# Kernel tuning notes

Hardware: AMD Instinct MI355X
Metric: run time of the kernel (lower is better)

The kernel has to match this reference:

```python
import jax, jax.numpy as jnp
import numpy as np

M, D_H, D_K, D_V = 8, 512, 64, 64
B, N = 16, 1024

def _xavier(key, shape, gain=1.414):
    fan_in, fan_out = shape[-2], shape[-1]
    limit = gain * (6.0 / (fan_in + fan_out)) ** 0.5
    return jax.random.uniform(key, shape, jnp.float32, -limit, limit)

def setup_inputs() -> dict:
    key = jax.random.key(0)
    kH, kq, kk, kv, ko = jax.random.split(key, 5)
    return {
        "H": jax.random.normal(kH, (B, N, D_H), jnp.float32),
        "W_Q": _xavier(kq, (M, D_H, D_K)),
        "W_K": _xavier(kk, (M, D_H, D_K)),
        "W_V": _xavier(kv, (M, D_H, D_V)),
        "W_O": _xavier(ko, (M, D_V, D_H)),
    }

def reference(H, W_Q, W_K, W_V, W_O):
    # H: [B, n, d_h]; per-head projections -> [B, M, n, d_k/d_v]
    Q = jnp.einsum('bnd,mdq->bmnq', H, W_Q)
    K = jnp.einsum('bnd,mdk->bmnk', H, W_K)
    V = jnp.einsum('bnd,mdv->bmnv', H, W_V)
    scale = 1.0 / jnp.sqrt(jnp.float32(W_K.shape[-1]))
    U = scale * jnp.einsum('bmnq,bmkq->bmnk', Q, K)  # [B, M, n, n]
    A = jax.nn.softmax(U, axis=-1)
    Hp = jnp.einsum('bmnk,bmkv->bmnv', A, V)          # [B, M, n, d_v]
    # per-head output projection then sum over heads (dim=-3)
    return jnp.einsum('bmnv,mvd->bnd', Hp, W_O)       # [B, n, d_h]
```

## Files before the change

kernel.cpp:

```cpp
#include <hip/hip_runtime.h>
#include <hip/hip_bf16.h>

typedef __attribute__((ext_vector_type(8))) short bf16x8;
typedef __attribute__((ext_vector_type(4))) float f32x4;
typedef __attribute__((ext_vector_type(16))) float f32x16;
typedef __attribute__((ext_vector_type(2))) unsigned uint2v;

__device__ __forceinline__ ushort f2bf(float f) {
  union { float f; unsigned u; } v; v.f = f;
  unsigned r = v.u + 0x7FFFu + ((v.u >> 16) & 1u);
  return (ushort)(r >> 16);
}

__device__ __forceinline__ float exp2_(float x) {
#if __has_builtin(__builtin_amdgcn_exp2f)
  return __builtin_amdgcn_exp2f(x);
#else
  return exp2f(x);
#endif
}

__device__ __forceinline__ unsigned cvtpk(float lo, float hi) {
  unsigned r;
  asm("v_cvt_pk_bf16_f32 %0, %1, %2" : "=v"(r) : "v"(lo), "v"(hi));
  return r;
}

__device__ __forceinline__ uint2v lane32_swap(unsigned a, unsigned b) {
#if __has_builtin(__builtin_amdgcn_permlane32_swap)
  return __builtin_amdgcn_permlane32_swap(a, b, false, false);
#else
  unsigned sa = (unsigned)__shfl_xor((int)a, 32);
  unsigned sb = (unsigned)__shfl_xor((int)b, 32);
  bool lo = ((threadIdx.x & 32) == 0);
  uint2v r;
  r.x = lo ? a : sb;
  r.y = lo ? sa : b;
  return r;
#endif
}

__device__ __forceinline__ void gload_lds16(const ushort* g, ushort* l) {
  __builtin_amdgcn_global_load_lds(
      (const __attribute__((address_space(1))) void*)g,
      (__attribute__((address_space(3))) void*)l, 16, 0, 0);
}

#define QSCALE 0.18033688011112042f

__global__ void __launch_bounds__(256) prep_kernel(
    const float* __restrict__ H, const float* __restrict__ WQ,
    const float* __restrict__ WK, const float* __restrict__ WV,
    const float* __restrict__ WO, ushort* __restrict__ Hb,
    ushort* __restrict__ Wqkv, ushort* __restrict__ Wo) {
  int bid = blockIdx.x;
  if (bid < 4096) {
    int i = (bid * 256 + threadIdx.x) * 8;
    float4 a = *(const float4*)(H + i);
    float4 b = *(const float4*)(H + i + 4);
    uint4 o;
    o.x = f2bf(a.x) | ((unsigned)f2bf(a.y) << 16);
    o.y = f2bf(a.z) | ((unsigned)f2bf(a.w) << 16);
    o.z = f2bf(b.x) | ((unsigned)f2bf(b.y) << 16);
    o.w = f2bf(b.z) | ((unsigned)f2bf(b.w) << 16);
    *(uint4*)(Hb + i) = o;
  } else if (bid < 7168) {
    int t = (bid - 4096) * 256 + threadIdx.x;
    int j = t >> 9, d = t & 511;
    int m = j / 192, r = j % 192, which = r >> 6, dk = r & 63;
    const float* W = (which == 0) ? WQ : (which == 1) ? WK : WV;
    Wqkv[t] = f2bf(W[(m * 512 + d) * 64 + dk]);
  } else {
    int t = (bid - 7168) * 256 + threadIdx.x;
    int j = t >> 9, mv = t & 511;
    Wo[t] = f2bf(WO[mv * 512 + j]);
  }
}

template <int EPI>
__global__ void __launch_bounds__(256) gemm_bt_kernel(
    const ushort* __restrict__ A, const ushort* __restrict__ Bt,
    float* __restrict__ C, int Kdim, int Ncols,
    ushort* __restrict__ Qo, ushort* __restrict__ Ko, ushort* __restrict__ Vo) {
  __shared__ __align__(16) ushort As[128 * 64];
  __shared__ __align__(16) ushort Bs[128 * 64];
  const int tid = threadIdx.x;
  const int lane = tid & 63, w = tid >> 6;
  const int wr = w >> 1, wc = w & 1;
  const int brow = blockIdx.y * 128, bcol = blockIdx.x * 128;

  const int srow = w * 32 + (lane >> 3);
  const int scol = (lane & 7) * 8;
  const ushort* ga = A + (size_t)(brow + srow) * Kdim + scol;
  const ushort* gb = Bt + (size_t)(bcol + srow) * Kdim + scol;

  f32x4 acc[4][4];
  const f32x4 z4 = {0.f, 0.f, 0.f, 0.f};
#pragma unroll
  for (int i = 0; i < 4; ++i)
#pragma unroll
    for (int j = 0; j < 4; ++j) acc[i][j] = z4;

  for (int k0 = 0; k0 < Kdim; k0 += 64) {
    __syncthreads();
#pragma unroll
    for (int t = 0; t < 4; ++t) {
      gload_lds16(ga + k0 + t * 8 * Kdim, &As[(w * 32 + t * 8) * 64]);
      gload_lds16(gb + k0 + t * 8 * Kdim, &Bs[(w * 32 + t * 8) * 64]);
    }
    __syncthreads();
#pragma unroll
    for (int kk = 0; kk < 64; kk += 32) {
      bf16x8 a[4], b[4];
#pragma unroll
      for (int i = 0; i < 4; ++i)
        a[i] = *(const bf16x8*)&As[(wr * 64 + i * 16 + (lane & 15)) * 64 + kk + (lane >> 4) * 8];
#pragma unroll
      for (int j = 0; j < 4; ++j)
        b[j] = *(const bf16x8*)&Bs[(wc * 64 + j * 16 + (lane & 15)) * 64 + kk + (lane >> 4) * 8];
#pragma unroll
      for (int i = 0; i < 4; ++i)
#pragma unroll
        for (int j = 0; j < 4; ++j)
          acc[i][j] = __builtin_amdgcn_mfma_f32_16x16x32_bf16(a[i], b[j], acc[i][j], 0, 0, 0);
    }
  }

#pragma unroll
  for (int i = 0; i < 4; ++i) {
    int row0 = brow + wr * 64 + i * 16 + (lane >> 4) * 4;
#pragma unroll
    for (int j = 0; j < 4; ++j) {
      int col = bcol + wc * 64 + j * 16 + (lane & 15);
      if (EPI == 0) {
#pragma unroll
        for (int q = 0; q < 4; ++q)
          C[(size_t)(row0 + q) * Ncols + col] = acc[i][j][q];
      } else {
        int m = col / 192, r = col % 192, which = r >> 6, dk = r & 63;
        ushort* base = (which == 0) ? Qo : (which == 1) ? Ko : Vo;
        float cs = (which == 0) ? QSCALE : 1.0f;
#pragma unroll
        for (int q = 0; q < 4; ++q) {
          int row = row0 + q;
          int bb = row >> 10, n = row & 1023;
          base[(size_t)((bb * 8 + m) * 1024 + n) * 64 + dk] = f2bf(acc[i][j][q] * cs);
        }
      }
    }
  }
}

__global__ void __launch_bounds__(256) transpose_v_kernel(const ushort* __restrict__ V,
                                                          ushort* __restrict__ Vt) {
  __shared__ __align__(16) ushort T[64][72];
  int bm = blockIdx.x >> 4, nt = blockIdx.x & 15;
  const ushort* src = V + (size_t)bm * 65536 + nt * 64 * 64;
  int tid = threadIdx.x;
#pragma unroll
  for (int i = 0; i < 2; ++i) {
    int c = tid + i * 256;
    int row = c >> 3, cc = (c & 7) * 8;
    *(uint4*)&T[row][cc] = *(const uint4*)(src + c * 8);
  }
  __syncthreads();
  int v = tid >> 2, nn0 = (tid & 3) * 16;
  ushort tmp[16];
#pragma unroll
  for (int k = 0; k < 16; ++k) tmp[k] = T[nn0 + k][v];
  ushort* dst = Vt + (size_t)bm * 65536 + v * 1024 + nt * 64 + nn0;
  *(uint4*)(dst + 0) = *(uint4*)&tmp[0];
  *(uint4*)(dst + 8) = *(uint4*)&tmp[8];
}

__global__ void __launch_bounds__(256, 2) attn_kernel(const ushort* __restrict__ Q,
                                                      const ushort* __restrict__ K,
                                                      const ushort* __restrict__ Vt,
                                                      ushort* __restrict__ Hp) {
  __shared__ __align__(16) ushort Ks[2][64 * 64];
  __shared__ __align__(16) ushort Vs[2][64 * 64];

  int wk = (blockIdx.x & 7) * 64 + (blockIdx.x >> 3);
  const int bm = wk >> 2, qt = wk & 3;
  const int b = bm >> 3, m = bm & 7;
  const int tid = threadIdx.x, lane = tid & 63, w = tid >> 6;
  const int hi = lane >> 5, l31 = lane & 31;
  const ushort* Qp = Q + (size_t)bm * 65536;
  const ushort* Kp = K + (size_t)bm * 65536;
  const ushort* Vp = Vt + (size_t)bm * 65536;
  const int qw = qt * 256 + w * 64;

  bf16x8 qb[2][4];
#pragma unroll
  for (int qs = 0; qs < 2; ++qs)
#pragma unroll
    for (int s = 0; s < 4; ++s)
      qb[qs][s] = *(const bf16x8*)(Qp + (size_t)(qw + qs * 32 + l31) * 64 + s * 16 + hi * 8);

  bf16x8 ones;
#pragma unroll
  for (int j = 0; j < 8; ++j) ones[j] = (short)0x3F80;

  f32x16 oacc[2][2], lacc[2];
#pragma unroll
  for (int r = 0; r < 16; ++r) {
    oacc[0][0][r] = 0.f; oacc[0][1][r] = 0.f;
    oacc[1][0][r] = 0.f; oacc[1][1][r] = 0.f;
    lacc[0][r] = 0.f; lacc[1][r] = 0.f;
  }

  const int sr = tid >> 2, sc4 = (tid & 3) << 4;
  const unsigned bo0 = ((unsigned)(sc4 * 2)) ^ (((unsigned)(sr & 7)) << 4);

  {
    uint4 k0 = *(const uint4*)(Kp + (size_t)sr * 64 + sc4);
    uint4 k1 = *(const uint4*)(Kp + (size_t)sr * 64 + sc4 + 8);
    uint4 v0 = *(const uint4*)(Vp + (size_t)sr * 1024 + sc4);
    uint4 v1 = *(const uint4*)(Vp + (size_t)sr * 1024 + sc4 + 8);
    char* kd = (char*)&Ks[0][sr * 64];
    char* vd = (char*)&Vs[0][sr * 64];
    *(uint4*)(kd + bo0) = k0; *(uint4*)(kd + (bo0 ^ 16)) = k1;
    *(uint4*)(vd + bo0) = v0; *(uint4*)(vd + (bo0 ^ 16)) = v1;
  }
  __syncthreads();

  int cur = 0;
  for (int kt = 0; kt < 16; ++kt) {
    uint4 k0, k1, v0, v1;
    const bool pf = (kt < 15);
    if (pf) {
      int n0 = (kt + 1) * 64;
      k0 = *(const uint4*)(Kp + (size_t)(n0 + sr) * 64 + sc4);
      k1 = *(const uint4*)(Kp + (size_t)(n0 + sr) * 64 + sc4 + 8);
      v0 = *(const uint4*)(Vp + (size_t)sr * 1024 + n0 + sc4);
      v1 = *(const uint4*)(Vp + (size_t)sr * 1024 + n0 + sc4 + 8);
    }

    const ushort* kbase = &Ks[cur][0];
    bf16x8 kA[2][4];
#pragma unroll
    for (int ja = 0; ja < 2; ++ja) {
      int row = ja * 32 + l31;
      const char* kr = (const char*)(kbase + row * 64);
#pragma unroll
      for (int s = 0; s < 4; ++s)
        kA[ja][s] = *(const bf16x8*)(kr + (((unsigned)(s * 32 + hi * 16)) ^ (((unsigned)(row & 7)) << 4)));
    }

    f32x16 st[2][2];
#pragma unroll
    for (int qs = 0; qs < 2; ++qs)
#pragma unroll
      for (int ja = 0; ja < 2; ++ja) {
#pragma unroll
        for (int r = 0; r < 16; ++r) st[qs][ja][r] = 0.f;
#pragma unroll
        for (int s = 0; s < 4; ++s)
          st[qs][ja] = __builtin_amdgcn_mfma_f32_32x32x16_bf16(kA[ja][s], qb[qs][s], st[qs][ja], 0, 0, 0);
      }

    bf16x8 pb[2][4];
#pragma unroll
    for (int qs = 0; qs < 2; ++qs) {
#pragma unroll
      for (int r = 0; r < 16; ++r) {
        st[qs][0][r] = exp2_(st[qs][0][r]);
        st[qs][1][r] = exp2_(st[qs][1][r]);
      }

#pragma unroll
      for (int ja = 0; ja < 2; ++ja) {
#pragma unroll
        for (int g = 0; g < 2; ++g) {
          unsigned x0 = cvtpk(st[qs][ja][g * 8 + 0], st[qs][ja][g * 8 + 1]);
          unsigned x1 = cvtpk(st[qs][ja][g * 8 + 2], st[qs][ja][g * 8 + 3]);
          unsigned y0 = cvtpk(st[qs][ja][g * 8 + 4], st[qs][ja][g * 8 + 5]);
          unsigned y1 = cvtpk(st[qs][ja][g * 8 + 6], st[qs][ja][g * 8 + 7]);
          uint2v s0 = lane32_swap(x0, y0);
          uint2v s1 = lane32_swap(x1, y1);
          uint4 wv; wv.x = s0.x; wv.y = s1.x; wv.z = s0.y; wv.w = s1.y;
          pb[qs][ja * 2 + g] = *(bf16x8*)&wv;
        }
      }

#pragma unroll
      for (int ks = 0; ks < 4; ++ks)
        lacc[qs] = __builtin_amdgcn_mfma_f32_32x32x16_bf16(ones, pb[qs][ks], lacc[qs], 0, 0, 0);
    }

    const ushort* vbase = &Vs[cur][0];
#pragma unroll
    for (int vj = 0; vj < 2; ++vj) {
      int row = vj * 32 + l31;
      const char* vr = (const char*)(vbase + row * 64);
      bf16x8 va[4];
#pragma unroll
      for (int ks = 0; ks < 4; ++ks)
        va[ks] = *(const bf16x8*)(vr + (((unsigned)(ks * 32 + hi * 16)) ^ (((unsigned)(row & 7)) << 4)));
#pragma unroll
      for (int qs = 0; qs < 2; ++qs)
#pragma unroll
        for (int ks = 0; ks < 4; ++ks)
          oacc[qs][vj] = __builtin_amdgcn_mfma_f32_32x32x16_bf16(va[ks], pb[qs][ks], oacc[qs][vj], 0, 0, 0);
    }

    if (pf) {
      char* kd = (char*)&Ks[cur ^ 1][sr * 64];
      char* vd = (char*)&Vs[cur ^ 1][sr * 64];
      *(uint4*)(kd + bo0) = k0; *(uint4*)(kd + (bo0 ^ 16)) = k1;
      *(uint4*)(vd + bo0) = v0; *(uint4*)(vd + (bo0 ^ 16)) = v1;
    }
    __syncthreads();
    cur ^= 1;
  }

#pragma unroll
  for (int qs = 0; qs < 2; ++qs) {
    float linv = 1.0f / lacc[qs][0];
    int q = qw + qs * 32 + l31;
    size_t ro = ((size_t)b * 1024 + q) * 512 + m * 64;
#pragma unroll
    for (int vj = 0; vj < 2; ++vj)
#pragma unroll
      for (int t4 = 0; t4 < 4; ++t4) {
        ushort4 o;
        o.x = f2bf(oacc[qs][vj][t4 * 4 + 0] * linv);
        o.y = f2bf(oacc[qs][vj][t4 * 4 + 1] * linv);
        o.z = f2bf(oacc[qs][vj][t4 * 4 + 2] * linv);
        o.w = f2bf(oacc[qs][vj][t4 * 4 + 3] * linv);
        *(ushort4*)(Hp + ro + vj * 32 + t4 * 8 + hi * 4) = o;
      }
  }
}

extern "C" void kernel_launch(void* const* d_in, const int* in_sizes, int n_in,
                              void* d_out, int out_size, void* d_ws, size_t ws_size,
                              hipStream_t stream) {
  const float* H  = (const float*)d_in[0];
  const float* WQ = (const float*)d_in[1];
  const float* WK = (const float*)d_in[2];
  const float* WV = (const float*)d_in[3];
  const float* WO = (const float*)d_in[4];
  float* out = (float*)d_out;

  ushort* ws   = (ushort*)d_ws;
  ushort* Hb   = ws;
  ushort* Wqkv = Hb + 16384 * 512;
  ushort* Wo   = Wqkv + 1536 * 512;
  ushort* Qb   = Wo + 512 * 512;
  ushort* Kb   = Qb + 128 * 1024 * 64;
  ushort* Vb   = Kb + 128 * 1024 * 64;
  ushort* Vtb  = Vb + 128 * 1024 * 64;
  ushort* Hp   = Vtb + 128 * 1024 * 64;

  prep_kernel<<<8192, 256, 0, stream>>>(H, WQ, WK, WV, WO, Hb, Wqkv, Wo);
  gemm_bt_kernel<1><<<dim3(12, 128), 256, 0, stream>>>(Hb, Wqkv, nullptr, 512, 1536,
                                                       Qb, Kb, Vb);
  transpose_v_kernel<<<2048, 256, 0, stream>>>(Vb, Vtb);
  attn_kernel<<<512, 256, 0, stream>>>(Qb, Kb, Vtb, Hp);
  gemm_bt_kernel<0><<<dim3(4, 128), 256, 0, stream>>>(Hp, Wo, out, 512, 512,
                                                      nullptr, nullptr, nullptr);
}
```

Baseline: 130.2 us.

## Pipeline bf16 GEMMs with double-buffered LDS, XOR swizzle and block remap

Replaces the single-buffered GEMM with a double-buffered pipeline. Each 64-wide K tile is split into two 32-wide halves, and the global-to-LDS load for the next half is issued while MFMAs run on the current one, with explicit vmcnt waits, barriers and priority raises. LDS slots are XOR-swizzled to reduce bank conflicts, and workgroup ids are remapped across 8 groups to change L2 locality. The unrolled loop hardcodes Kdim=512 (8 tiles), and the doubled LDS use together with launch bounds of 2 may limit occupancy.

Result: faster. 117.0 us, median of 2 (-10.1%).

```diff
diff --git a/kernel.cpp b/kernel.cpp
--- a/kernel.cpp
+++ b/kernel.cpp
@@ -44,6 +44,11 @@
   __builtin_amdgcn_global_load_lds(
       (const __attribute__((address_space(1))) void*)g,
       (__attribute__((address_space(3))) void*)l, 16, 0, 0);
+}
+
+template <int N>
+__device__ __forceinline__ void vmw() {
+  asm volatile("s_waitcnt vmcnt(%0)" ::"i"(N) : "memory");
 }
 
 #define QSCALE 0.18033688011112042f
@@ -78,21 +83,28 @@
 }
 
 template <int EPI>
-__global__ void __launch_bounds__(256) gemm_bt_kernel(
+__global__ void __launch_bounds__(256, 2) gemm_bt_pipe(
     const ushort* __restrict__ A, const ushort* __restrict__ Bt,
     float* __restrict__ C, int Kdim, int Ncols,
     ushort* __restrict__ Qo, ushort* __restrict__ Ko, ushort* __restrict__ Vo) {
-  __shared__ __align__(16) ushort As[128 * 64];
-  __shared__ __align__(16) ushort Bs[128 * 64];
-  const int tid = threadIdx.x;
-  const int lane = tid & 63, w = tid >> 6;
-  const int wr = w >> 1, wc = w & 1;
-  const int brow = blockIdx.y * 128, bcol = blockIdx.x * 128;
-
-  const int srow = w * 32 + (lane >> 3);
-  const int scol = (lane & 7) * 8;
-  const ushort* ga = A + (size_t)(brow + srow) * Kdim + scol;
-  const ushort* gb = Bt + (size_t)(bcol + srow) * Kdim + scol;
+  __shared__ __align__(16) ushort S[32768];
+  ushort* SA = S;
+  ushort* SB = S + 16384;
+
+  const int tid = threadIdx.x, lane = tid & 63, w = tid >> 6;
+  const int hi = lane >> 4, l15 = lane & 15, l3 = lane & 3;
+  const int wm = w >> 1, wn = w & 1;
+
+  const int gx = gridDim.x;
+  const int nwg = gx * gridDim.y;
+  const int bid = blockIdx.y * gx + blockIdx.x;
+  const int id2 = (bid & 7) * (nwg >> 3) + (bid >> 3);
+  const int brow = (id2 / gx) * 128, bcol = (id2 % gx) * 128;
+
+  const int srow = w * 32 + (lane >> 2);
+  const int sslot = ((lane & 3) ^ ((lane >> 2) & 3)) * 8;
+  const ushort* aS = A + (size_t)(brow + srow) * Kdim + sslot;
+  const ushort* bS = Bt + (size_t)(bcol + srow) * Kdim + sslot;
 
   f32x4 acc[4][4];
   const f32x4 z4 = {0.f, 0.f, 0.f, 0.f};
@@ -101,37 +113,83 @@
 #pragma unroll
     for (int j = 0; j < 4; ++j) acc[i][j] = z4;
 
-  for (int k0 = 0; k0 < Kdim; k0 += 64) {
-    __syncthreads();
-#pragma unroll
-    for (int t = 0; t < 4; ++t) {
-      gload_lds16(ga + k0 + t * 8 * Kdim, &As[(w * 32 + t * 8) * 64]);
-      gload_lds16(gb + k0 + t * 8 * Kdim, &Bs[(w * 32 + t * 8) * 64]);
-    }
-    __syncthreads();
-#pragma unroll
-    for (int kk = 0; kk < 64; kk += 32) {
-      bf16x8 a[4], b[4];
-#pragma unroll
-      for (int i = 0; i < 4; ++i)
-        a[i] = *(const bf16x8*)&As[(wr * 64 + i * 16 + (lane & 15)) * 64 + kk + (lane >> 4) * 8];
+  auto STAGE = [&](int T, int h, int buf) {
+    const ushort* a0 = aS + T * 64 + h * 32;
+    const ushort* b0 = bS + T * 64 + h * 32;
+    ushort* la = SA + buf * 8192 + h * 4096 + (w * 32) * 32;
+    ushort* lb = SB + buf * 8192 + h * 4096 + (w * 32) * 32;
+    gload_lds16(a0, la);
+    gload_lds16(a0 + (size_t)16 * Kdim, la + 512);
+    gload_lds16(b0, lb);
+    gload_lds16(b0 + (size_t)16 * Kdim, lb + 512);
+  };
+
+  auto LOADF = [&](int buf, int h, bf16x8* af, bf16x8* bf) {
+    const ushort* Ab = SA + buf * 8192 + h * 4096;
+    const ushort* Bb = SB + buf * 8192 + h * 4096;
+#pragma unroll
+    for (int fr = 0; fr < 4; ++fr) {
+      int r = wm * 64 + fr * 16 + l15;
+      af[fr] = *(const bf16x8*)&Ab[r * 32 + ((hi ^ l3) << 3)];
+    }
+#pragma unroll
+    for (int fc = 0; fc < 4; ++fc) {
+      int r = wn * 64 + fc * 16 + l15;
+      bf[fc] = *(const bf16x8*)&Bb[r * 32 + ((hi ^ l3) << 3)];
+    }
+  };
+
+  auto MFMA16 = [&](bf16x8* af, bf16x8* bf) {
+#pragma unroll
+    for (int i = 0; i < 4; ++i)
 #pragma unroll
       for (int j = 0; j < 4; ++j)
-        b[j] = *(const bf16x8*)&Bs[(wc * 64 + j * 16 + (lane & 15)) * 64 + kk + (lane >> 4) * 8];
-#pragma unroll
-      for (int i = 0; i < 4; ++i)
-#pragma unroll
-        for (int j = 0; j < 4; ++j)
-          acc[i][j] = __builtin_amdgcn_mfma_f32_16x16x32_bf16(a[i], b[j], acc[i][j], 0, 0, 0);
+        acc[i][j] = __builtin_amdgcn_mfma_f32_16x16x32_bf16(af[i], bf[j], acc[i][j], 0, 0, 0);
+  };
+
+  STAGE(0, 0, 0);
+  STAGE(0, 1, 0);
+  STAGE(1, 0, 1);
+  vmw<8>();
+  __builtin_amdgcn_s_barrier();
+
+#pragma unroll
+  for (int t = 0; t < 8; ++t) {
+    const int buf = t & 1;
+    {
+      bf16x8 af[4], bf[4];
+      LOADF(buf, 0, af, bf);
+      if (t < 7) STAGE(t + 1, 1, buf ^ 1);
+      if (t < 7) vmw<8>(); else vmw<0>();
+      __builtin_amdgcn_s_barrier();
+      asm volatile("s_waitcnt lgkmcnt(0)" ::: "memory");
+      __builtin_amdgcn_sched_barrier(0);
+      __builtin_amdgcn_s_setprio(1);
+      MFMA16(af, bf);
+      __builtin_amdgcn_s_setprio(0);
+      __builtin_amdgcn_s_barrier();
+    }
+    {
+      bf16x8 af[4], bf[4];
+      LOADF(buf, 1, af, bf);
+      if (t < 6) STAGE(t + 2, 0, buf);
+      if (t < 6) vmw<8>(); else if (t == 6) vmw<4>(); else vmw<0>();
+      __builtin_amdgcn_s_barrier();
+      asm volatile("s_waitcnt lgkmcnt(0)" ::: "memory");
+      __builtin_amdgcn_sched_barrier(0);
+      __builtin_amdgcn_s_setprio(1);
+      MFMA16(af, bf);
+      __builtin_amdgcn_s_setprio(0);
+      __builtin_amdgcn_s_barrier();
     }
   }
 
 #pragma unroll
   for (int i = 0; i < 4; ++i) {
-    int row0 = brow + wr * 64 + i * 16 + (lane >> 4) * 4;
+    int row0 = brow + wm * 64 + i * 16 + hi * 4;
 #pragma unroll
     for (int j = 0; j < 4; ++j) {
-      int col = bcol + wc * 64 + j * 16 + (lane & 15);
+      int col = bcol + wn * 64 + j * 16 + l15;
       if (EPI == 0) {
 #pragma unroll
         for (int q = 0; q < 4; ++q)
@@ -354,10 +412,10 @@
   ushort* Hp   = Vtb + 128 * 1024 * 64;
 
   prep_kernel<<<8192, 256, 0, stream>>>(H, WQ, WK, WV, WO, Hb, Wqkv, Wo);
-  gemm_bt_kernel<1><<<dim3(12, 128), 256, 0, stream>>>(Hb, Wqkv, nullptr, 512, 1536,
-                                                       Qb, Kb, Vb);
+  gemm_bt_pipe<1><<<dim3(12, 128), 256, 0, stream>>>(Hb, Wqkv, nullptr, 512, 1536,
+                                                     Qb, Kb, Vb);
   transpose_v_kernel<<<2048, 256, 0, stream>>>(Vb, Vtb);
   attn_kernel<<<512, 256, 0, stream>>>(Qb, Kb, Vtb, Hp);
-  gemm_bt_kernel<0><<<dim3(4, 128), 256, 0, stream>>>(Hp, Wo, out, 512, 512,
-                                                      nullptr, nullptr, nullptr);
-}
+  gemm_bt_pipe<0><<<dim3(4, 128), 256, 0, stream>>>(Hp, Wo, out, 512, 512,
+                                                    nullptr, nullptr, nullptr);
+}
```
